# Kernel optimization log

Measured on AMD Instinct MI355X. Metric: run time of the kernel, lower is better.

The kernel has to match this reference:

```python
import jax, jax.numpy as jnp
import numpy as np

N_ATOMS = 10000
N_PAIRS = 100000
H = 64          # hidden_channels
R = 32          # number_of_radial_basis_functions
MAX_Z = 100
CUTOFF = 0.5    # nm (radial_max_distance), min = 0.0


def cosine_cutoff(d):
    # 0.5*(cos(pi*d/rc)+1) for d < rc else 0
    return jnp.where(d < CUTOFF, 0.5 * (jnp.cos(jnp.pi * d / CUTOFF) + 1.0), 0.0)


def expnormal_rbf(d):
    # ExpNormal smearing (TorchMD/TensorNet style), cutoff_lower = 0
    start = float(np.exp(-CUTOFF))
    means = jnp.linspace(start, 1.0, R, dtype=d.dtype)            # [R]
    beta = (2.0 / R * (1.0 - start)) ** -2
    alpha = 5.0 / CUTOFF
    return jnp.exp(-beta * (jnp.exp(-alpha * d)[:, None] - means) ** 2)  # [P,R]


def vector_to_skewtensor(v):
    x, y, z = v[:, 0], v[:, 1], v[:, 2]
    o = jnp.zeros_like(x)
    return jnp.stack([o, -z, y, z, o, -x, -y, x, o], axis=-1).reshape(-1, 3, 3)


def vector_to_symtensor(v):
    t = v[:, :, None] * v[:, None, :]                              # [P,3,3]
    tr3 = (t[:, 0, 0] + t[:, 1, 1] + t[:, 2, 2]) / 3.0
    return t - tr3[:, None, None] * jnp.eye(3, dtype=v.dtype)


def setup_inputs() -> dict:
    key = jax.random.key(0)
    ks = jax.random.split(key, 20)
    atomic_numbers = jax.random.randint(ks[0], (N_ATOMS,), 0, MAX_Z)
    pair_indices = jax.random.randint(ks[1], (2, N_PAIRS), 0, N_ATOMS)
    r_ij = jax.random.normal(ks[2], (N_PAIRS, 3), dtype=jnp.float32) * 0.12  # ~0.2 nm norms
    d_ij = jnp.linalg.norm(r_ij, axis=-1, keepdims=True) + 1e-6
    s = 0.1
    p = {
        'emb':    jax.random.normal(ks[3], (MAX_Z, H)) * s,
        'emb2_w': jax.random.normal(ks[4], (H, 2 * H)) * s,
        'emb2_b': jnp.zeros((H,)),
        'dp1_w':  jax.random.normal(ks[5], (H, R)) * s,
        'dp1_b':  jnp.zeros((H,)),
        'dp2_w':  jax.random.normal(ks[6], (H, R)) * s,
        'dp2_b':  jnp.zeros((H,)),
        'dp3_w':  jax.random.normal(ks[7], (H, R)) * s,
        'dp3_b':  jnp.zeros((H,)),
        'lt0_w':  jax.random.normal(ks[8], (H, H)) * s,
        'lt1_w':  jax.random.normal(ks[9], (H, H)) * s,
        'lt2_w':  jax.random.normal(ks[10], (H, H)) * s,
        'ls1_w':  jax.random.normal(ks[11], (2 * H, H)) * s,
        'ls1_b':  jnp.zeros((2 * H,)),
        'ls2_w':  jax.random.normal(ks[12], (3 * H, 2 * H)) * s,
        'ls2_b':  jnp.zeros((3 * H,)),
        'ln_g':   jnp.ones((H,)),
        'ln_b':   jnp.zeros((H,)),
    }
    return dict(atomic_numbers=atomic_numbers, pair_indices=pair_indices,
                d_ij=d_ij, r_ij=r_ij, **p)


def reference(atomic_numbers, pair_indices, d_ij, r_ij,
              emb, emb2_w, emb2_b, dp1_w, dp1_b, dp2_w, dp2_b, dp3_w, dp3_b,
              lt0_w, lt1_w, lt2_w, ls1_w, ls1_b, ls2_w, ls2_b, ln_g, ln_b):
    n_atoms = atomic_numbers.shape[0]
    src = pair_indices[0]
    # atomic number message Zij: concat(emb[i], emb[j]) -> Linear
    zi = emb[atomic_numbers]                                      # [N,H]
    zij = jnp.concatenate([zi[src], zi[pair_indices[1]]], axis=-1)  # [P,2H]
    Zij = zij @ emb2_w.T + emb2_b                                 # [P,H]
    d = d_ij[:, 0]                                                # [P]
    unit = r_ij / d_ij                                            # [P,3]
    rc = cosine_cutoff(d)                                         # [P]
    rbf = expnormal_rbf(d) * rc[:, None]                          # [P,R]
    C = rc[:, None] * Zij                                         # [P,H]
    f1 = (rbf @ dp1_w.T + dp1_b) * C                              # [P,H]
    f2 = (rbf @ dp2_w.T + dp2_b) * C * 10.0                       # Angstrom scale
    f3 = (rbf @ dp3_w.T + dp3_b) * C * 100.0
    eye = jnp.eye(3, dtype=r_ij.dtype)
    skew = vector_to_skewtensor(unit)                             # [P,3,3]
    sym = vector_to_symtensor(unit)                               # [P,3,3]
    Iij = f1[:, :, None, None] * eye                              # [P,H,3,3]
    Aij = f2[:, :, None, None] * skew[:, None]
    Sij = f3[:, :, None, None] * sym[:, None]
    I = jax.ops.segment_sum(Iij, src, num_segments=n_atoms)       # [N,H,3,3]
    A = jax.ops.segment_sum(Aij, src, num_segments=n_atoms)
    S = jax.ops.segment_sum(Sij, src, num_segments=n_atoms)
    # tensor_norm -> LayerNorm -> scalar MLP
    tn = jnp.sum((I + A + S) ** 2, axis=(-2, -1))                 # [N,H]
    mu = tn.mean(-1, keepdims=True)
    var = tn.var(-1, keepdims=True)
    norm = (tn - mu) / jnp.sqrt(var + 1e-5) * ln_g + ln_b
    norm = jax.nn.silu(norm @ ls1_w.T + ls1_b)
    norm = jax.nn.silu(norm @ ls2_w.T + ls2_b)                    # [N,3H]
    norm = norm.reshape(-1, H, 3)
    I = jnp.einsum('nhij,gh->ngij', I, lt0_w) * norm[:, :, 0][:, :, None, None]
    A = jnp.einsum('nhij,gh->ngij', A, lt1_w) * norm[:, :, 1][:, :, None, None]
    S = jnp.einsum('nhij,gh->ngij', S, lt2_w) * norm[:, :, 2][:, :, None, None]
    return I + A + S
```

## Files before the change

kernel.cpp:

```cpp
#include <hip/hip_runtime.h>
#include <hip/hip_bf16.h>

#define N_ATOMS 10000
#define N_PAIRS 100000
#define HH 64
#define MAXZ 100

typedef _Float16 h2_t __attribute__((ext_vector_type(2)));

constexpr float RBF_START = 0.6065306597126334f;
constexpr float RBF_STEP  = (1.0f - RBF_START) / 31.0f;
constexpr float RBF_BETA  = 1.0f / ((0.0625f * (1.0f - RBF_START)) * (0.0625f * (1.0f - RBF_START)));
constexpr float LOG2E     = 1.4426950408889634f;
constexpr float NEG_ALPHA_L2 = -10.0f * LOG2E;
constexpr float NEG_BETA_L2  = -RBF_BETA * LOG2E;

#define OFF_EMB   0
#define OFF_W2    6400
#define OFF_B2    14592
#define OFF_D1W   14656
#define OFF_D1B   16704
#define OFF_D2W   16768
#define OFF_D2B   18816
#define OFF_D3W   18880
#define OFF_D3B   20928
#define OFF_LT0   20992
#define OFF_LT1   25088
#define OFF_LT2   29184
#define OFF_L1W   33280
#define OFF_L1B   41472
#define OFF_L2W   41600
#define OFF_L2B   66176
#define OFF_LNG   66368
#define OFF_LNB   66432
#define N_PARAMF  66496

#define PH_DP   0
#define PH_L1   3072
#define PH_L2   7168
#define PH_LT   19456
#define PH_N    25600

#define WS_WF     0
#define WS_CNT    266240
#define WS_OFF    307200
#define WS_CUR    348160
#define WS_T1     389120
#define WS_T2     414720
#define WS_PH     440320
#define WS_DPK    542720
#define WS_ZNL    2142720
#define WS_ACCH   2542720

__device__ __forceinline__ float bf2f(unsigned short u) {
    return __uint_as_float(((unsigned int)u) << 16);
}
__device__ __forceinline__ float fexp2(float x) { return __builtin_amdgcn_exp2f(x); }
__device__ __forceinline__ float fcos2pi(float x) { return __builtin_amdgcn_cosf(x); }
__device__ __forceinline__ float fsilu(float x) { return x / (1.0f + fexp2(-LOG2E * x)); }
__device__ __forceinline__ h2_t u2h(unsigned u) { return __builtin_bit_cast(h2_t, u); }
__device__ __forceinline__ unsigned packh2(float a, float b) {
    h2_t v; v.x = (_Float16)a; v.y = (_Float16)b;
    return __builtin_bit_cast(unsigned, v);
}

#if __has_builtin(__builtin_amdgcn_fdot2)
__device__ __forceinline__ float FDOT2(h2_t a, h2_t b, float c) {
    return __builtin_amdgcn_fdot2(a, b, c, false);
}
#else
__device__ __forceinline__ float FDOT2(h2_t a, h2_t b, float c) {
    return c + (float)a.x * (float)b.x + (float)a.y * (float)b.y;
}
#endif
__device__ __forceinline__ float dot16h(const uint4* w, const uint4* x, float acc) {
    uint4 a = *w, b = *x;
    acc = FDOT2(u2h(a.x), u2h(b.x), acc);
    acc = FDOT2(u2h(a.y), u2h(b.y), acc);
    acc = FDOT2(u2h(a.z), u2h(b.z), acc);
    acc = FDOT2(u2h(a.w), u2h(b.w), acc);
    return acc;
}

__device__ int classify64(const unsigned short* b, int lane) {
    unsigned short x = b[lane];
    int e = (x >> 7) & 0xFF;
    bool implaus = (x != 0) && (e < 96 || e > 133);
    bool zeroeven = ((lane & 1) == 0) && (x == 0);
    unsigned long long mi = __ballot(implaus);
    unsigned long long mz = __ballot(zeroeven);
    if (__popcll(mz) == 32) return 0;
    if (__popcll(mi) >= 8) return 0;
    return 1;
}

struct ConvArgs { const void* src[18]; float* dst; };

__global__ void k_prep(ConvArgs a, const int* __restrict__ pidx, int* __restrict__ cnt) {
    const int sizes[18] = {6400,8192,64,2048,64,2048,64,2048,64,4096,4096,4096,8192,128,24576,192,64,64};
    __shared__ int fl;
    if (threadIdx.x < 64) {
        int f = classify64((const unsigned short*)a.src[0], threadIdx.x);
        if (threadIdx.x == 0) fl = f;
    }
    __syncthreads();
    int t = blockIdx.x * 256 + threadIdx.x;
    if (t < N_PARAMF) {
        int acc = 0, seg = 0, off = t;
        #pragma unroll
        for (int i = 0; i < 18; ++i) {
            if (t >= acc && t < acc + sizes[i]) { seg = i; off = t - acc; }
            acc += sizes[i];
        }
        if (fl == 1) a.dst[t] = bf2f(((const unsigned short*)a.src[seg])[off]);
        else         a.dst[t] = ((const float*)a.src[seg])[off];
    }
    if (t < N_PAIRS) atomicAdd(&cnt[pidx[t]], 1);
}

__global__ void k_tabpack(const float* __restrict__ WF, float* __restrict__ T1,
                          float* __restrict__ T2, unsigned* __restrict__ PH) {
    int z = blockIdx.x;
    int h = threadIdx.x;
    if (h < 64) {
        const float* ez = WF + OFF_EMB + z * HH;
        const float* w2 = WF + OFF_W2 + h * 128;
        float s1 = 0.f, s2 = 0.f;
        #pragma unroll
        for (int k = 0; k < 64; ++k) {
            float e = ez[k];
            s1 += w2[k] * e;
            s2 += w2[64 + k] * e;
        }
        T1[z * HH + h] = s1;
        T2[z * HH + h] = s2;
    }
    int q = blockIdx.x * 256 + threadIdx.x;
    int src;
    if (q < PH_L1) {
        int w = q >> 10, r = q & 1023;
        src = (w == 0 ? OFF_D1W : (w == 1 ? OFF_D2W : OFF_D3W)) + r * 2;
    } else if (q < PH_L2) {
        src = OFF_L1W + (q - PH_L1) * 2;
    } else if (q < PH_LT) {
        src = OFF_L2W + (q - PH_L2) * 2;
    } else {
        src = OFF_LT0 + (q - PH_LT) * 2;
    }
    PH[q] = packh2(WF[src], WF[src + 1]);
}

__global__ void k_scan(const int* __restrict__ cnt, int* __restrict__ offs, int* __restrict__ cur) {
    __shared__ int buf[1024];
    int tid = threadIdx.x;
    int base = tid * 10;
    int c[10]; int s = 0;
    #pragma unroll
    for (int i = 0; i < 10; ++i) {
        int idx = base + i;
        int v = (idx < N_ATOMS) ? cnt[idx] : 0;
        c[i] = v; s += v;
    }
    buf[tid] = s;
    __syncthreads();
    for (int off = 1; off < 1024; off <<= 1) {
        int v = (tid >= off) ? buf[tid - off] : 0;
        __syncthreads();
        buf[tid] += v;
        __syncthreads();
    }
    int run = buf[tid] - s;
    #pragma unroll
    for (int i = 0; i < 10; ++i) {
        int idx = base + i;
        if (idx < N_ATOMS) { offs[idx] = run; cur[idx] = run; run += c[i]; }
    }
    if (tid == 0) offs[N_ATOMS] = N_PAIRS;
}

__global__ void k_fill(const int* __restrict__ pidx, const int* __restrict__ an,
                       const void* __restrict__ dij_v, const void* __restrict__ rij_v,
                       int* __restrict__ cur,
                       float4* __restrict__ dpack, int* __restrict__ znl) {
    __shared__ int fdr[2];
    if (threadIdx.x < 64) {
        int fd = classify64((const unsigned short*)dij_v, threadIdx.x);
        int fr = classify64((const unsigned short*)rij_v, threadIdx.x);
        if (threadIdx.x == 0) { fdr[0] = fd; fdr[1] = fr; }
    }
    __syncthreads();
    int p = blockIdx.x * 256 + threadIdx.x;
    if (p >= N_PAIRS) return;
    int s = pidx[p];
    int dst = pidx[N_PAIRS + p];
    int pos = atomicAdd(&cur[s], 1);
    float d, rx, ry, rz;
    if (fdr[0] == 1) d = bf2f(((const unsigned short*)dij_v)[p]);
    else             d = ((const float*)dij_v)[p];
    if (fdr[1] == 1) {
        const unsigned short* r = (const unsigned short*)rij_v;
        rx = bf2f(r[3*p]); ry = bf2f(r[3*p+1]); rz = bf2f(r[3*p+2]);
    } else {
        const float* r = (const float*)rij_v;
        rx = r[3*p]; ry = r[3*p+1]; rz = r[3*p+2];
    }
    dpack[pos] = make_float4(rx, ry, rz, d);
    znl[pos] = an[dst];
}

__global__ __launch_bounds__(256, 4) void k_pair(
    const int* __restrict__ an,
    const float* __restrict__ WF,
    const int* __restrict__ offs,
    const float4* __restrict__ dpack, const int* __restrict__ znl,
    const float* __restrict__ T1, const float* __restrict__ T2,
    const unsigned* __restrict__ PH,
    unsigned* __restrict__ accH)
{
    __shared__ __align__(16) unsigned dpL[3 * 1280];
    __shared__ __align__(16) unsigned rbq[4 * 16];

    for (int q = threadIdx.x; q < 3072; q += 256) {
        int w = q >> 10, r = q & 1023;
        int hh = r >> 4, u = r & 15;
        dpL[w * 1280 + hh * 20 + u] = PH[PH_DP + q];
    }
    __syncthreads();

    const int wave = threadIdx.x >> 6;
    const int h    = threadIdx.x & 63;
    const int n    = blockIdx.x * 4 + wave;

    _Float16* rbfh = (_Float16*)&rbq[wave * 16];
    const uint4* w1p = (const uint4*)&dpL[0 * 1280 + h * 20];
    const uint4* w2p = (const uint4*)&dpL[1 * 1280 + h * 20];
    const uint4* w3p = (const uint4*)&dpL[2 * 1280 + h * 20];
    const uint4* rbp = (const uint4*)&rbq[wave * 16];

    const float ed1 = (WF + OFF_D1B)[h];
    const float ed2 = (WF + OFF_D2B)[h];
    const float ed3 = (WF + OFF_D3B)[h];
    const float zA  = (WF + OFF_B2)[h] + T1[an[n] * HH + h];

    float Is=0.f, sx=0.f, sy=0.f, sz=0.f;
    float Sxx=0.f, Syy=0.f, Szz=0.f, Sxy=0.f, Sxz=0.f, Syz=0.f;

    const int pbeg = offs[n], pend = offs[n + 1];

    float4 dp_cur = make_float4(0.f, 0.f, 0.f, 1.f);
    float  t2cur  = 0.f;
    int    zn_n   = 0;
    if (pbeg < pend) {
        dp_cur = dpack[pbeg];
        t2cur  = T2[znl[pbeg] * HH + h];
        if (pbeg + 1 < pend) zn_n = znl[pbeg + 1];
    }

    for (int ii = pbeg; ii < pend; ++ii) {
        const float4 dpv = dp_cur;
        const float  t2v = t2cur;
        if (ii + 1 < pend) {
            dp_cur = dpack[ii + 1];
            t2cur  = T2[zn_n * HH + h];
            if (ii + 2 < pend) zn_n = znl[ii + 2];
        }

        float d = dpv.w;
        float inv = 1.0f / d;
        float ux = dpv.x*inv, uy = dpv.y*inv, uz = dpv.z*inv;
        float rc = (d < 0.5f) ? 0.5f * (fcos2pi(d) + 1.0f) : 0.0f;

        if (h < 32) {
            float en = fexp2(NEG_ALPHA_L2 * d);
            float t = en - (RBF_START + RBF_STEP * (float)h);
            rbfh[h] = (_Float16)(fexp2(NEG_BETA_L2 * t * t) * rc);
        }
        __builtin_amdgcn_wave_barrier();

        float g1 = ed1, g2 = ed2, g3 = ed3;
        #pragma unroll
        for (int k = 0; k < 4; ++k) {
            g1 = dot16h(w1p + k, rbp + k, g1);
            g2 = dot16h(w2p + k, rbp + k, g2);
            g3 = dot16h(w3p + k, rbp + k, g3);
        }

        float zc = zA + t2v;
        float Cc = rc * zc;
        float f1 = g1 * Cc;
        float f2 = g2 * Cc * 10.0f;
        float f3 = g3 * Cc * 100.0f;

        Is += f1;
        sx += f2 * ux;  sy += f2 * uy;  sz += f2 * uz;
        float q = (ux*ux + uy*uy + uz*uz) * (1.0f / 3.0f);
        Sxx += f3 * (ux*ux - q);
        Syy += f3 * (uy*uy - q);
        Szz += f3 * (uz*uz - q);
        Sxy += f3 * (ux*uy);
        Sxz += f3 * (ux*uz);
        Syz += f3 * (uy*uz);
        __builtin_amdgcn_wave_barrier();
    }

    float tn = 3.0f*Is*Is + 2.0f*(sx*sx + sy*sy + sz*sz)
             + Sxx*Sxx + Syy*Syy + Szz*Szz
             + 2.0f*(Sxy*Sxy + Sxz*Sxz + Syz*Syz);
    float s1 = tn, s2 = tn * tn;
    #pragma unroll
    for (int o = 32; o > 0; o >>= 1) {
        s1 += __shfl_xor(s1, o);
        s2 += __shfl_xor(s2, o);
    }
    float mu  = s1 * (1.0f / 64.0f);
    float var = s2 * (1.0f / 64.0f) - mu * mu;
    float nv  = (tn - mu) * rsqrtf(var + 1e-5f) * (WF + OFF_LNG)[h] + (WF + OFF_LNB)[h];

    float vals[11] = {Is, sx, sy, sz, Sxx, Syy, Szz, Sxy, Sxz, Syz, nv};
    #pragma unroll
    for (int c = 0; c < 11; ++c) {
        float pv = __shfl_xor(vals[c], 1);
        if ((h & 1) == 0)
            accH[((n * 11 + c) << 5) + (h >> 1)] = packh2(vals[c], pv);
    }
}

__global__ __launch_bounds__(256, 2) void k_post(
    const float* __restrict__ WF,
    const unsigned* __restrict__ PH,
    const unsigned* __restrict__ accH,
    float* __restrict__ out)
{
    __shared__ __align__(16) unsigned wL2[192 * 68];
    __shared__ __align__(16) unsigned acch[4][12 * 32];
    __shared__ __align__(16) unsigned y1h[4][64];
    __shared__ __align__(16) unsigned y2h[4][96];

    for (int q = threadIdx.x; q < 12288; q += 256) {
        int m = q >> 6, u = q & 63;
        wL2[m * 68 + u] = PH[PH_L2 + q];
    }
    __syncthreads();

    const int wave = threadIdx.x >> 6;
    const int h    = threadIdx.x & 63;
    const int gw   = blockIdx.x * 4 + wave;
    const int GW   = gridDim.x * 4;

    const uint4* l1base = (const uint4*)(PH + PH_L1);
    const uint4* lt0 = (const uint4*)(PH + PH_LT) + h * 8;
    const uint4* lt1 = (const uint4*)(PH + PH_LT + 2048) + h * 8;
    const uint4* lt2 = (const uint4*)(PH + PH_LT + 4096) + h * 8;

    for (int n = gw; n < N_ATOMS; n += GW) {
        if (h < 32) {
            #pragma unroll
            for (int c = 0; c < 11; ++c)
                acch[wave][c * 32 + h] = accH[((n * 11 + c) << 5) + h];
        }
        __builtin_amdgcn_wave_barrier();

        const uint4* nvh = (const uint4*)&acch[wave][10 * 32];

        float ya = (WF + OFF_L1B)[h];
        float yb = (WF + OFF_L1B)[h + 64];
        {
            const uint4* ra = l1base + h * 8;
            const uint4* rb = l1base + (h + 64) * 8;
            #pragma unroll
            for (int k = 0; k < 8; ++k) {
                ya = dot16h(ra + k, nvh + k, ya);
                yb = dot16h(rb + k, nvh + k, yb);
            }
        }
        ya = fsilu(ya); yb = fsilu(yb);
        {
            float pa = __shfl_xor(ya, 1);
            float pb = __shfl_xor(yb, 1);
            if ((h & 1) == 0) {
                y1h[wave][(h >> 1)]      = packh2(ya, pa);
                y1h[wave][32 + (h >> 1)] = packh2(yb, pb);
            }
        }
        __builtin_amdgcn_wave_barrier();

        const uint4* y1p = (const uint4*)&y1h[wave][0];
        float z0 = (WF + OFF_L2B)[h];
        float z1 = (WF + OFF_L2B)[h + 64];
        float z2 = (WF + OFF_L2B)[h + 128];
        {
            const uint4* r0 = (const uint4*)&wL2[(h)       * 68];
            const uint4* r1 = (const uint4*)&wL2[(h + 64)  * 68];
            const uint4* r2 = (const uint4*)&wL2[(h + 128) * 68];
            #pragma unroll
            for (int k = 0; k < 16; ++k) {
                uint4 x = y1p[k];
                uint4 a0 = r0[k], a1 = r1[k], a2 = r2[k];
                z0 = FDOT2(u2h(a0.x), u2h(x.x), z0); z0 = FDOT2(u2h(a0.y), u2h(x.y), z0);
                z0 = FDOT2(u2h(a0.z), u2h(x.z), z0); z0 = FDOT2(u2h(a0.w), u2h(x.w), z0);
                z1 = FDOT2(u2h(a1.x), u2h(x.x), z1); z1 = FDOT2(u2h(a1.y), u2h(x.y), z1);
                z1 = FDOT2(u2h(a1.z), u2h(x.z), z1); z1 = FDOT2(u2h(a1.w), u2h(x.w), z1);
                z2 = FDOT2(u2h(a2.x), u2h(x.x), z2); z2 = FDOT2(u2h(a2.y), u2h(x.y), z2);
                z2 = FDOT2(u2h(a2.z), u2h(x.z), z2); z2 = FDOT2(u2h(a2.w), u2h(x.w), z2);
            }
        }
        z0 = fsilu(z0); z1 = fsilu(z1); z2 = fsilu(z2);
        {
            float p0 = __shfl_xor(z0, 1);
            float p1 = __shfl_xor(z1, 1);
            float p2 = __shfl_xor(z2, 1);
            if ((h & 1) == 0) {
                y2h[wave][(h >> 1)]      = packh2(z0, p0);
                y2h[wave][32 + (h >> 1)] = packh2(z1, p1);
                y2h[wave][64 + (h >> 1)] = packh2(z2, p2);
            }
        }
        __builtin_amdgcn_wave_barrier();

        float n0, n1, n2;
        {
            int i0 = 3 * h;
            unsigned u0 = y2h[wave][i0 >> 1];
            unsigned u1 = y2h[wave][(i0 >> 1) + 1];
            h2_t a = u2h(u0), b = u2h(u1);
            if (i0 & 1) { n0 = (float)a.y; n1 = (float)b.x; n2 = (float)b.y; }
            else        { n0 = (float)a.x; n1 = (float)a.y; n2 = (float)b.x; }
        }

        const uint4* aI  = (const uint4*)&acch[wave][0];
        const uint4* aAx = (const uint4*)&acch[wave][32];
        const uint4* aAy = (const uint4*)&acch[wave][64];
        const uint4* aAz = (const uint4*)&acch[wave][96];
        const uint4* aXX = (const uint4*)&acch[wave][128];
        const uint4* aYY = (const uint4*)&acch[wave][160];
        const uint4* aZZ = (const uint4*)&acch[wave][192];
        const uint4* aXY = (const uint4*)&acch[wave][224];
        const uint4* aXZ = (const uint4*)&acch[wave][256];
        const uint4* aYZ = (const uint4*)&acch[wave][288];

        float P0=0.f, PAx=0.f, PAy=0.f, PAz=0.f;
        float Q0=0.f, Q1=0.f, Q2=0.f, Q3=0.f, Q4=0.f, Q5=0.f;
        #pragma unroll
        for (int k = 0; k < 8; ++k) {
            P0  = dot16h(lt0 + k, aI  + k, P0);
            PAx = dot16h(lt1 + k, aAx + k, PAx);
            PAy = dot16h(lt1 + k, aAy + k, PAy);
            PAz = dot16h(lt1 + k, aAz + k, PAz);
            Q0  = dot16h(lt2 + k, aXX + k, Q0);
            Q1  = dot16h(lt2 + k, aYY + k, Q1);
            Q2  = dot16h(lt2 + k, aZZ + k, Q2);
            Q3  = dot16h(lt2 + k, aXY + k, Q3);
            Q4  = dot16h(lt2 + k, aXZ + k, Q4);
            Q5  = dot16h(lt2 + k, aYZ + k, Q5);
        }
        float Iv = P0 * n0;
        float Ax = PAx * n1, Ay = PAy * n1, Az = PAz * n1;
        float Xx = Q0 * n2, Yy = Q1 * n2, Zz = Q2 * n2;
        float Xy = Q3 * n2, Xz = Q4 * n2, Yz = Q5 * n2;

        float* o = out + (size_t)n * 576 + h * 9;
        o[0] =  Iv + Xx;  o[1] = -Az + Xy;  o[2] =  Ay + Xz;
        o[3] =  Az + Xy;  o[4] =  Iv + Yy;  o[5] = -Ax + Yz;
        o[6] = -Ay + Xz;  o[7] =  Ax + Yz;  o[8] =  Iv + Zz;
        __builtin_amdgcn_wave_barrier();
    }
}

extern "C" void kernel_launch(void* const* d_in, const int* in_sizes, int n_in,
                              void* d_out, int out_size, void* d_ws, size_t ws_size,
                              hipStream_t stream) {
    const int* an   = (const int*)d_in[0];
    const int* pidx = (const int*)d_in[1];

    char* ws = (char*)d_ws;
    float*    WF    = (float*)(ws + WS_WF);
    int*      cnt   = (int*)(ws + WS_CNT);
    int*      offs  = (int*)(ws + WS_OFF);
    int*      cur   = (int*)(ws + WS_CUR);
    float*    T1    = (float*)(ws + WS_T1);
    float*    T2    = (float*)(ws + WS_T2);
    unsigned* PH    = (unsigned*)(ws + WS_PH);
    float4*   dpack = (float4*)(ws + WS_DPK);
    int*      znl   = (int*)(ws + WS_ZNL);
    unsigned* accH  = (unsigned*)(ws + WS_ACCH);
    float*    out   = (float*)d_out;

    hipMemsetAsync(cnt, 0, N_ATOMS * sizeof(int), stream);

    ConvArgs ca;
    for (int i = 0; i < 18; ++i) ca.src[i] = d_in[4 + i];
    ca.dst = WF;
    k_prep<<<(N_PAIRS + 255) / 256, 256, 0, stream>>>(ca, pidx, cnt);
    k_tabpack<<<100, 256, 0, stream>>>(WF, T1, T2, PH);
    k_scan<<<1, 1024, 0, stream>>>(cnt, offs, cur);
    k_fill<<<(N_PAIRS + 255) / 256, 256, 0, stream>>>(pidx, an, d_in[2], d_in[3],
                                                      cur, dpack, znl);
    k_pair<<<2500, 256, 0, stream>>>(an, WF, offs, dpack, znl, T1, T2, PH, accH);
    k_post<<<256, 256, 0, stream>>>(WF, PH, accH, out);
}
```

Baseline: 209.9 us.

## Precompute per-pair RBF and unit vectors in fill; merge scan and table kernels

Moves the per-pair radial basis, cosine cutoff and unit-vector computation out of the per-atom wave loop and into the k_fill kernel. It stores 32 fp16 RBF values per pair in a new workspace buffer, and k_pair now streams them and keeps the distance-projection weights in registers instead of LDS. This removes wave barriers and redundant per-lane transcendental work. The scan and table-pack kernels are merged into one launch to save a launch. It adds about 6.4 MB of extra global traffic, reduces the occupancy hint on k_pair from 4 to 2, and doubles the k_post grid.

```diff
diff --git a/kernel.cpp b/kernel.cpp
--- a/kernel.cpp
+++ b/kernel.cpp
@@ -50,7 +50,8 @@
 #define WS_PH     440320
 #define WS_DPK    542720
 #define WS_ZNL    2142720
-#define WS_ACCH   2542720
+#define WS_RBF    2542720
+#define WS_ACCH   8942720
 
 __device__ __forceinline__ float bf2f(unsigned short u) {
     return __uint_as_float(((unsigned int)u) << 16);
@@ -73,13 +74,15 @@
     return c + (float)a.x * (float)b.x + (float)a.y * (float)b.y;
 }
 #endif
-__device__ __forceinline__ float dot16h(const uint4* w, const uint4* x, float acc) {
-    uint4 a = *w, b = *x;
+__device__ __forceinline__ float dot16v(uint4 a, uint4 b, float acc) {
     acc = FDOT2(u2h(a.x), u2h(b.x), acc);
     acc = FDOT2(u2h(a.y), u2h(b.y), acc);
     acc = FDOT2(u2h(a.z), u2h(b.z), acc);
     acc = FDOT2(u2h(a.w), u2h(b.w), acc);
     return acc;
+}
+__device__ __forceinline__ float dot16h(const uint4* w, const uint4* x, float acc) {
+    return dot16v(*w, *x, acc);
 }
 
 __device__ int classify64(const unsigned short* b, int lane) {
@@ -118,11 +121,41 @@
     if (t < N_PAIRS) atomicAdd(&cnt[pidx[t]], 1);
 }
 
-__global__ void k_tabpack(const float* __restrict__ WF, float* __restrict__ T1,
-                          float* __restrict__ T2, unsigned* __restrict__ PH) {
-    int z = blockIdx.x;
-    int h = threadIdx.x;
-    if (h < 64) {
+__global__ void k_scantab(const float* __restrict__ WF, float* __restrict__ T1,
+                          float* __restrict__ T2, unsigned* __restrict__ PH,
+                          const int* __restrict__ cnt, int* __restrict__ offs,
+                          int* __restrict__ cur) {
+    __shared__ int buf[1024];
+    if (blockIdx.x == 0) {
+        int tid = threadIdx.x;
+        int base = tid * 10;
+        int c[10]; int s = 0;
+        #pragma unroll
+        for (int i = 0; i < 10; ++i) {
+            int idx = base + i;
+            int v = (idx < N_ATOMS) ? cnt[idx] : 0;
+            c[i] = v; s += v;
+        }
+        buf[tid] = s;
+        __syncthreads();
+        for (int off = 1; off < 1024; off <<= 1) {
+            int v = (tid >= off) ? buf[tid - off] : 0;
+            __syncthreads();
+            buf[tid] += v;
+            __syncthreads();
+        }
+        int run = buf[tid] - s;
+        #pragma unroll
+        for (int i = 0; i < 10; ++i) {
+            int idx = base + i;
+            if (idx < N_ATOMS) { offs[idx] = run; cur[idx] = run; run += c[i]; }
+        }
+        if (tid == 0) offs[N_ATOMS] = N_PAIRS;
+        return;
+    }
+    int t = (blockIdx.x - 1) * 1024 + threadIdx.x;
+    if (t < 6400) {
+        int z = t >> 6, h = t & 63;
         const float* ez = WF + OFF_EMB + z * HH;
         const float* w2 = WF + OFF_W2 + h * 128;
         float s1 = 0.f, s2 = 0.f;
@@ -135,53 +168,27 @@
         T1[z * HH + h] = s1;
         T2[z * HH + h] = s2;
     }
-    int q = blockIdx.x * 256 + threadIdx.x;
-    int src;
-    if (q < PH_L1) {
-        int w = q >> 10, r = q & 1023;
-        src = (w == 0 ? OFF_D1W : (w == 1 ? OFF_D2W : OFF_D3W)) + r * 2;
-    } else if (q < PH_L2) {
-        src = OFF_L1W + (q - PH_L1) * 2;
-    } else if (q < PH_LT) {
-        src = OFF_L2W + (q - PH_L2) * 2;
-    } else {
-        src = OFF_LT0 + (q - PH_LT) * 2;
-    }
-    PH[q] = packh2(WF[src], WF[src + 1]);
-}
-
-__global__ void k_scan(const int* __restrict__ cnt, int* __restrict__ offs, int* __restrict__ cur) {
-    __shared__ int buf[1024];
-    int tid = threadIdx.x;
-    int base = tid * 10;
-    int c[10]; int s = 0;
-    #pragma unroll
-    for (int i = 0; i < 10; ++i) {
-        int idx = base + i;
-        int v = (idx < N_ATOMS) ? cnt[idx] : 0;
-        c[i] = v; s += v;
-    }
-    buf[tid] = s;
-    __syncthreads();
-    for (int off = 1; off < 1024; off <<= 1) {
-        int v = (tid >= off) ? buf[tid - off] : 0;
-        __syncthreads();
-        buf[tid] += v;
-        __syncthreads();
-    }
-    int run = buf[tid] - s;
-    #pragma unroll
-    for (int i = 0; i < 10; ++i) {
-        int idx = base + i;
-        if (idx < N_ATOMS) { offs[idx] = run; cur[idx] = run; run += c[i]; }
-    }
-    if (tid == 0) offs[N_ATOMS] = N_PAIRS;
+    if (t < PH_N) {
+        int src;
+        if (t < PH_L1) {
+            int w = t >> 10, r = t & 1023;
+            src = (w == 0 ? OFF_D1W : (w == 1 ? OFF_D2W : OFF_D3W)) + r * 2;
+        } else if (t < PH_L2) {
+            src = OFF_L1W + (t - PH_L1) * 2;
+        } else if (t < PH_LT) {
+            src = OFF_L2W + (t - PH_L2) * 2;
+        } else {
+            src = OFF_LT0 + (t - PH_LT) * 2;
+        }
+        PH[t] = packh2(WF[src], WF[src + 1]);
+    }
 }
 
 __global__ void k_fill(const int* __restrict__ pidx, const int* __restrict__ an,
                        const void* __restrict__ dij_v, const void* __restrict__ rij_v,
                        int* __restrict__ cur,
-                       float4* __restrict__ dpack, int* __restrict__ znl) {
+                       float4* __restrict__ dpack, int* __restrict__ znl,
+                       unsigned* __restrict__ rbfp) {
     __shared__ int fdr[2];
     if (threadIdx.x < 64) {
         int fd = classify64((const unsigned short*)dij_v, threadIdx.x);
@@ -204,38 +211,43 @@
         const float* r = (const float*)rij_v;
         rx = r[3*p]; ry = r[3*p+1]; rz = r[3*p+2];
     }
-    dpack[pos] = make_float4(rx, ry, rz, d);
+    float inv = 1.0f / d;
+    float rc = (d < 0.5f) ? 0.5f * (fcos2pi(d) + 1.0f) : 0.0f;
+    dpack[pos] = make_float4(rx * inv, ry * inv, rz * inv, rc);
     znl[pos] = an[dst];
-}
-
-__global__ __launch_bounds__(256, 4) void k_pair(
+    float en = fexp2(NEG_ALPHA_L2 * d);
+    unsigned* rp = rbfp + pos * 16;
+    #pragma unroll
+    for (int r2 = 0; r2 < 16; ++r2) {
+        float t0 = en - (RBF_START + RBF_STEP * (float)(2 * r2));
+        float t1 = en - (RBF_START + RBF_STEP * (float)(2 * r2 + 1));
+        float v0 = fexp2(NEG_BETA_L2 * t0 * t0) * rc;
+        float v1 = fexp2(NEG_BETA_L2 * t1 * t1) * rc;
+        rp[r2] = packh2(v0, v1);
+    }
+}
+
+__global__ __launch_bounds__(256, 2) void k_pair(
     const int* __restrict__ an,
     const float* __restrict__ WF,
     const int* __restrict__ offs,
     const float4* __restrict__ dpack, const int* __restrict__ znl,
+    const unsigned* __restrict__ rbfp,
     const float* __restrict__ T1, const float* __restrict__ T2,
     const unsigned* __restrict__ PH,
     unsigned* __restrict__ accH)
 {
-    __shared__ __align__(16) unsigned dpL[3 * 1280];
-    __shared__ __align__(16) unsigned rbq[4 * 16];
-
-    for (int q = threadIdx.x; q < 3072; q += 256) {
-        int w = q >> 10, r = q & 1023;
-        int hh = r >> 4, u = r & 15;
-        dpL[w * 1280 + hh * 20 + u] = PH[PH_DP + q];
-    }
-    __syncthreads();
-
     const int wave = threadIdx.x >> 6;
     const int h    = threadIdx.x & 63;
     const int n    = blockIdx.x * 4 + wave;
 
-    _Float16* rbfh = (_Float16*)&rbq[wave * 16];
-    const uint4* w1p = (const uint4*)&dpL[0 * 1280 + h * 20];
-    const uint4* w2p = (const uint4*)&dpL[1 * 1280 + h * 20];
-    const uint4* w3p = (const uint4*)&dpL[2 * 1280 + h * 20];
-    const uint4* rbp = (const uint4*)&rbq[wave * 16];
+    const uint4* wp = (const uint4*)(PH + PH_DP);
+    const uint4 w10 = wp[        h * 4 + 0], w11 = wp[        h * 4 + 1],
+                w12 = wp[        h * 4 + 2], w13 = wp[        h * 4 + 3];
+    const uint4 w20 = wp[256 +   h * 4 + 0], w21 = wp[256 +   h * 4 + 1],
+                w22 = wp[256 +   h * 4 + 2], w23 = wp[256 +   h * 4 + 3];
+    const uint4 w30 = wp[512 +   h * 4 + 0], w31 = wp[512 +   h * 4 + 1],
+                w32 = wp[512 +   h * 4 + 2], w33 = wp[512 +   h * 4 + 3];
 
     const float ed1 = (WF + OFF_D1B)[h];
     const float ed2 = (WF + OFF_D2B)[h];
@@ -246,47 +258,42 @@
     float Sxx=0.f, Syy=0.f, Szz=0.f, Sxy=0.f, Sxz=0.f, Syz=0.f;
 
     const int pbeg = offs[n], pend = offs[n + 1];
-
-    float4 dp_cur = make_float4(0.f, 0.f, 0.f, 1.f);
-    float  t2cur  = 0.f;
-    int    zn_n   = 0;
+    const uint4* rbase = (const uint4*)rbfp;
+
+    float4 dp_cur = make_float4(0.f, 0.f, 0.f, 0.f);
+    uint4  r0c = {0,0,0,0}, r1c = {0,0,0,0}, r2c = {0,0,0,0}, r3c = {0,0,0,0};
+    float  t2cur = 0.f;
+    int    zn_n  = 0;
     if (pbeg < pend) {
         dp_cur = dpack[pbeg];
-        t2cur  = T2[znl[pbeg] * HH + h];
+        r0c = rbase[pbeg*4+0]; r1c = rbase[pbeg*4+1];
+        r2c = rbase[pbeg*4+2]; r3c = rbase[pbeg*4+3];
+        t2cur = T2[znl[pbeg] * HH + h];
         if (pbeg + 1 < pend) zn_n = znl[pbeg + 1];
     }
 
     for (int ii = pbeg; ii < pend; ++ii) {
         const float4 dpv = dp_cur;
+        const uint4  b0 = r0c, b1 = r1c, b2 = r2c, b3 = r3c;
         const float  t2v = t2cur;
         if (ii + 1 < pend) {
             dp_cur = dpack[ii + 1];
-            t2cur  = T2[zn_n * HH + h];
+            r0c = rbase[(ii+1)*4+0]; r1c = rbase[(ii+1)*4+1];
+            r2c = rbase[(ii+1)*4+2]; r3c = rbase[(ii+1)*4+3];
+            t2cur = T2[zn_n * HH + h];
             if (ii + 2 < pend) zn_n = znl[ii + 2];
         }
 
-        float d = dpv.w;
-        float inv = 1.0f / d;
-        float ux = dpv.x*inv, uy = dpv.y*inv, uz = dpv.z*inv;
-        float rc = (d < 0.5f) ? 0.5f * (fcos2pi(d) + 1.0f) : 0.0f;
-
-        if (h < 32) {
-            float en = fexp2(NEG_ALPHA_L2 * d);
-            float t = en - (RBF_START + RBF_STEP * (float)h);
-            rbfh[h] = (_Float16)(fexp2(NEG_BETA_L2 * t * t) * rc);
-        }
-        __builtin_amdgcn_wave_barrier();
-
         float g1 = ed1, g2 = ed2, g3 = ed3;
-        #pragma unroll
-        for (int k = 0; k < 4; ++k) {
-            g1 = dot16h(w1p + k, rbp + k, g1);
-            g2 = dot16h(w2p + k, rbp + k, g2);
-            g3 = dot16h(w3p + k, rbp + k, g3);
-        }
-
-        float zc = zA + t2v;
-        float Cc = rc * zc;
+        g1 = dot16v(w10, b0, g1); g1 = dot16v(w11, b1, g1);
+        g1 = dot16v(w12, b2, g1); g1 = dot16v(w13, b3, g1);
+        g2 = dot16v(w20, b0, g2); g2 = dot16v(w21, b1, g2);
+        g2 = dot16v(w22, b2, g2); g2 = dot16v(w23, b3, g2);
+        g3 = dot16v(w30, b0, g3); g3 = dot16v(w31, b1, g3);
+        g3 = dot16v(w32, b2, g3); g3 = dot16v(w33, b3, g3);
+
+        float ux = dpv.x, uy = dpv.y, uz = dpv.z, rc = dpv.w;
+        float Cc = rc * (zA + t2v);
         float f1 = g1 * Cc;
         float f2 = g2 * Cc * 10.0f;
         float f3 = g3 * Cc * 100.0f;
@@ -300,7 +307,6 @@
         Sxy += f3 * (ux*uy);
         Sxz += f3 * (ux*uz);
         Syz += f3 * (uy*uz);
-        __builtin_amdgcn_wave_barrier();
     }
 
     float tn = 3.0f*Is*Is + 2.0f*(sx*sx + sy*sy + sz*sz)
@@ -395,13 +401,9 @@
             #pragma unroll
             for (int k = 0; k < 16; ++k) {
                 uint4 x = y1p[k];
-                uint4 a0 = r0[k], a1 = r1[k], a2 = r2[k];
-                z0 = FDOT2(u2h(a0.x), u2h(x.x), z0); z0 = FDOT2(u2h(a0.y), u2h(x.y), z0);
-                z0 = FDOT2(u2h(a0.z), u2h(x.z), z0); z0 = FDOT2(u2h(a0.w), u2h(x.w), z0);
-                z1 = FDOT2(u2h(a1.x), u2h(x.x), z1); z1 = FDOT2(u2h(a1.y), u2h(x.y), z1);
-                z1 = FDOT2(u2h(a1.z), u2h(x.z), z1); z1 = FDOT2(u2h(a1.w), u2h(x.w), z1);
-                z2 = FDOT2(u2h(a2.x), u2h(x.x), z2); z2 = FDOT2(u2h(a2.y), u2h(x.y), z2);
-                z2 = FDOT2(u2h(a2.z), u2h(x.z), z2); z2 = FDOT2(u2h(a2.w), u2h(x.w), z2);
+                z0 = dot16v(r0[k], x, z0);
+                z1 = dot16v(r1[k], x, z1);
+                z2 = dot16v(r2[k], x, z2);
             }
         }
         z0 = fsilu(z0); z1 = fsilu(z1); z2 = fsilu(z2);
@@ -482,6 +484,7 @@
     unsigned* PH    = (unsigned*)(ws + WS_PH);
     float4*   dpack = (float4*)(ws + WS_DPK);
     int*      znl   = (int*)(ws + WS_ZNL);
+    unsigned* rbfp  = (unsigned*)(ws + WS_RBF);
     unsigned* accH  = (unsigned*)(ws + WS_ACCH);
     float*    out   = (float*)d_out;
 
@@ -491,10 +494,9 @@
     for (int i = 0; i < 18; ++i) ca.src[i] = d_in[4 + i];
     ca.dst = WF;
     k_prep<<<(N_PAIRS + 255) / 256, 256, 0, stream>>>(ca, pidx, cnt);
-    k_tabpack<<<100, 256, 0, stream>>>(WF, T1, T2, PH);
-    k_scan<<<1, 1024, 0, stream>>>(cnt, offs, cur);
+    k_scantab<<<26, 1024, 0, stream>>>(WF, T1, T2, PH, cnt, offs, cur);
     k_fill<<<(N_PAIRS + 255) / 256, 256, 0, stream>>>(pidx, an, d_in[2], d_in[3],
-                                                      cur, dpack, znl);
-    k_pair<<<2500, 256, 0, stream>>>(an, WF, offs, dpack, znl, T1, T2, PH, accH);
-    k_post<<<256, 256, 0, stream>>>(WF, PH, accH, out);
-}
+                                                      cur, dpack, znl, rbfp);
+    k_pair<<<2500, 256, 0, stream>>>(an, WF, offs, dpack, znl, rbfp, T1, T2, PH, accH);
+    k_post<<<512, 256, 0, stream>>>(WF, PH, accH, out);
+}
```

Result: no change. 210.4 us (+0.2%).
